# Performance work log

Measured on AMD Instinct MI355X. Metric: run time of the kernel, lower is better.

Reference implementation:

```python
import jax, jax.numpy as jnp
import numpy as np

EMBED_DIM = 768
N_HEADS = 12
HEAD_DIM = EMBED_DIM // N_HEADS


def setup_inputs() -> dict:
    key = jax.random.key(0)
    ks = jax.random.split(key, 6)
    bsz, seq = 2, 4096
    hidden_states = jax.random.normal(ks[0], (bsz, seq, EMBED_DIM), dtype=jnp.float32)
    attention_mask = jnp.zeros((bsz, 1, 1, seq), dtype=jnp.float32)
    s = 1.0 / np.sqrt(EMBED_DIM)
    Wq = jax.random.normal(ks[1], (EMBED_DIM, EMBED_DIM), dtype=jnp.float32) * s
    Wk = jax.random.normal(ks[2], (EMBED_DIM, EMBED_DIM), dtype=jnp.float32) * s
    Wv = jax.random.normal(ks[3], (EMBED_DIM, EMBED_DIM), dtype=jnp.float32) * s
    Wo = jax.random.normal(ks[4], (EMBED_DIM, EMBED_DIM), dtype=jnp.float32) * s
    bo = jax.random.normal(ks[5], (EMBED_DIM,), dtype=jnp.float32) * s
    return {"hidden_states": hidden_states, "attention_mask": attention_mask,
            "Wq": Wq, "Wk": Wk, "Wv": Wv, "Wo": Wo, "bo": bo}


def reference(hidden_states, attention_mask, Wq, Wk, Wv, Wo, bo):
    bsz, seq, _ = hidden_states.shape
    scale = 1.0 / np.sqrt(HEAD_DIM)

    def split_heads(x):  # [b, s, e] -> [b, h, s, d]
        return x.reshape(bsz, seq, N_HEADS, HEAD_DIM).transpose(0, 2, 1, 3)

    # nn.Linear applies x @ W.T
    q = split_heads(hidden_states @ Wq.T)
    k = split_heads(hidden_states @ Wk.T)
    v = split_heads(hidden_states @ Wv.T)

    # [b, h, tgt, src] score matrix (faithful to the bmm+softmax+bmm original)
    attn = jnp.einsum('bhqd,bhkd->bhqk', q, k) * scale
    attn = attn + attention_mask  # mask broadcasts [b,1,1,src]
    probs = jax.nn.softmax(attn, axis=-1)
    ctx = jnp.einsum('bhqk,bhkd->bhqd', probs, v)

    concat = ctx.transpose(0, 2, 1, 3).reshape(bsz, seq, EMBED_DIM)
    return concat @ Wo.T + bo
```

## Files before the change

### kernel.cpp

```cpp
#include <hip/hip_runtime.h>
#include <stdint.h>

#define ED   768
#define NH   12
#define HD   64
#define SEQ  4096
#define BSZ  2
#define BHT  (BSZ*NH)
#define MTOT (BSZ*SEQ)

typedef short bf16x8  __attribute__((ext_vector_type(8)));
typedef float f32x4   __attribute__((ext_vector_type(4)));
typedef float f32x16  __attribute__((ext_vector_type(16)));
typedef unsigned int u32x4 __attribute__((ext_vector_type(4)));

#define LOG2E 1.44269504088896340736f
#define C2    (0.125f * LOG2E)

__device__ __forceinline__ unsigned short f2bf(float f) {
    union { float f; uint32_t u; } v; v.f = f;
    uint32_t u = v.u;
    u += 0x7fffu + ((u >> 16) & 1u);
    return (unsigned short)(u >> 16);
}

__device__ __forceinline__ uint32_t cvtpk(float lo, float hi) {
    uint32_t r;
    asm("v_cvt_pk_bf16_f32 %0, %1, %2" : "=v"(r) : "v"(lo), "v"(hi));
    return r;
}

__device__ __forceinline__ void cp16(const unsigned short* g, unsigned short* l) {
    __builtin_amdgcn_global_load_lds(
        (const __attribute__((address_space(1))) unsigned int*)(const void*)g,
        (__attribute__((address_space(3))) unsigned int*)(void*)l,
        16, 0, 0);
}

#define H_CHUNKS  (MTOT * ED / 4)
#define W_CHUNKS  (ED * ED / 4)
#define CVT_TOTAL (H_CHUNKS + 4 * W_CHUNKS)

__global__ __launch_bounds__(256) void convert_bf16(
    const float* __restrict__ H,  const float* __restrict__ Wq,
    const float* __restrict__ Wk, const float* __restrict__ Wv,
    const float* __restrict__ Wo, unsigned short* __restrict__ dst,
    unsigned short* __restrict__ WoB) {
    int i4 = blockIdx.x * 256 + threadIdx.x;
    float4 v;
    ushort4* optr;
    if (i4 < H_CHUNKS) { v = ((const float4*)H)[i4]; optr = (ushort4*)dst + i4; }
    else {
        int j = i4 - H_CHUNKS;
        if (j < 3 * W_CHUNKS) {
            if (j < W_CHUNKS)          v = ((const float4*)Wq)[j];
            else if (j < 2 * W_CHUNKS) v = ((const float4*)Wk)[j - W_CHUNKS];
            else                       v = ((const float4*)Wv)[j - 2 * W_CHUNKS];
            optr = (ushort4*)dst + i4;
        } else {
            v = ((const float4*)Wo)[j - 3 * W_CHUNKS];
            optr = (ushort4*)WoB + (j - 3 * W_CHUNKS);
        }
    }
    ushort4 o;
    o.x = f2bf(v.x); o.y = f2bf(v.y); o.z = f2bf(v.z); o.w = f2bf(v.w);
    *optr = o;
}

__global__ __launch_bounds__(256) void qkv_gemm(
    const unsigned short* __restrict__ Hb,
    const unsigned short* __restrict__ Wb,
    unsigned short* __restrict__ qkv) {
    __shared__ __align__(16) unsigned short Ah[128 * 64];
    __shared__ __align__(16) unsigned short Bh[128 * 64];
    const int t = threadIdx.x, w = t >> 6, lane = t & 63;
    const int quad = lane >> 4, r16 = lane & 15;
    const int wm = w >> 1, wn = w & 1;
    const int m0 = blockIdx.y * 128, n0g = blockIdx.x * 128;
    const int wsel = n0g / ED, n0 = n0g % ED;
    const int lrow = lane >> 3;
    const int lchs = ((lane & 7) ^ (lrow & 7)) * 8;

    f32x4 acc[4][4] = {};
    for (int kt = 0; kt < ED / 64; ++kt) {
        const int k0 = kt * 64;
#pragma unroll
        for (int i = 0; i < 4; ++i) {
            int row = i * 32 + w * 8;
            cp16(&Hb[(size_t)(m0 + row + lrow) * ED + k0 + lchs], &Ah[row * 64]);
            cp16(&Wb[(size_t)(n0g + row + lrow) * ED + k0 + lchs], &Bh[row * 64]);
        }
        __syncthreads();
#pragma unroll
        for (int kk = 0; kk < 2; ++kk) {
            bf16x8 aF[4], bF[4];
#pragma unroll
            for (int mi = 0; mi < 4; ++mi) {
                int R = wm * 64 + mi * 16 + r16;
                aF[mi] = *(const bf16x8*)&Ah[R * 64 + (((kk * 4 + quad) ^ (r16 & 7)) * 8)];
            }
#pragma unroll
            for (int ni = 0; ni < 4; ++ni) {
                int R = wn * 64 + ni * 16 + r16;
                bF[ni] = *(const bf16x8*)&Bh[R * 64 + (((kk * 4 + quad) ^ (r16 & 7)) * 8)];
            }
            if (wsel == 2) {
#pragma unroll
                for (int mi = 0; mi < 4; ++mi)
#pragma unroll
                    for (int ni = 0; ni < 4; ++ni)
                        acc[mi][ni] = __builtin_amdgcn_mfma_f32_16x16x32_bf16(
                            bF[ni], aF[mi], acc[mi][ni], 0, 0, 0);
            } else {
#pragma unroll
                for (int mi = 0; mi < 4; ++mi)
#pragma unroll
                    for (int ni = 0; ni < 4; ++ni)
                        acc[mi][ni] = __builtin_amdgcn_mfma_f32_16x16x32_bf16(
                            aF[mi], bF[ni], acc[mi][ni], 0, 0, 0);
            }
        }
        __syncthreads();
    }
    const size_t WSZ = (size_t)BHT * SEQ * HD;
    if (wsel == 2) {
#pragma unroll
        for (int mi = 0; mi < 4; ++mi)
#pragma unroll
            for (int ni = 0; ni < 4; ++ni)
#pragma unroll
                for (int r = 0; r < 4; ++r) {
                    int m  = m0 + wm * 64 + mi * 16 + r16;
                    int nn = n0 + wn * 64 + ni * 16 + quad * 4 + r;
                    int b = m >> 12, s = m & 4095;
                    int hh = nn >> 6, dd = nn & 63;
                    qkv[2 * WSZ + (((size_t)b * NH + hh) * HD + dd) * SEQ + s] =
                        f2bf(acc[mi][ni][r]);
                }
    } else {
        const float sc = (wsel == 0) ? C2 : 1.0f;
#pragma unroll
        for (int mi = 0; mi < 4; ++mi)
#pragma unroll
            for (int ni = 0; ni < 4; ++ni)
#pragma unroll
                for (int r = 0; r < 4; ++r) {
                    int m = m0 + wm * 64 + mi * 16 + quad * 4 + r;
                    int b = m >> 12, s = m & 4095;
                    int nn = n0 + wn * 64 + ni * 16 + r16;
                    int hh = nn >> 6, dd = nn & 63;
                    size_t off = (((size_t)b * NH + hh) * SEQ + s) * HD + dd;
                    qkv[(size_t)wsel * WSZ + off] = f2bf(acc[mi][ni][r] * sc);
                }
    }
}

#define QK_PACK(KOFF, M0, M1, PF) do {                                         \
    float p_[2][16];                                                           \
    float rs0 = 0.f, rs1 = 0.f, rs2 = 0.f, rs3 = 0.f;                          \
_Pragma("unroll")                                                              \
    for (int st = 0; st < 2; ++st) {                                           \
        bf16x8 am = {};                                                        \
        if (hi == 0) am[0] = (short)f2bf(LOG2E * (st ? (M1) : (M0)));          \
        f32x16 sA = {};                                                        \
        sA = __builtin_amdgcn_mfma_f32_32x32x16_bf16(am, bOnes, sA, 0, 0, 0);  \
        __builtin_amdgcn_s_setprio(1);                                         \
_Pragma("unroll")                                                              \
        for (int kc = 0; kc < 4; ++kc) {                                       \
            bf16x8 kF = *(const bf16x8*)                                       \
                &Ksm[(KOFF) + (st * 32 + n31) * 64 + (((2 * kc + hi) ^ sw) * 8)]; \
            sA = __builtin_amdgcn_mfma_f32_32x32x16_bf16(kF, qF[kc], sA, 0, 0, 0); \
        }                                                                      \
        __builtin_amdgcn_s_setprio(0);                                         \
_Pragma("unroll")                                                              \
        for (int r = 0; r < 16; ++r) p_[st][r] = __builtin_amdgcn_exp2f(sA[r]); \
        rs0 += p_[st][0] + p_[st][4] + p_[st][8]  + p_[st][12];                \
        rs1 += p_[st][1] + p_[st][5] + p_[st][9]  + p_[st][13];                \
        rs2 += p_[st][2] + p_[st][6] + p_[st][10] + p_[st][14];                \
        rs3 += p_[st][3] + p_[st][7] + p_[st][11] + p_[st][15];                \
    }                                                                          \
    l_i += (rs0 + rs1) + (rs2 + rs3);                                          \
_Pragma("unroll")                                                              \
    for (int st = 0; st < 2; ++st) {                                           \
        uint32_t pw[8];                                                        \
_Pragma("unroll")                                                              \
        for (int i = 0; i < 8; ++i)                                            \
            pw[i] = cvtpk(p_[st][2 * i], p_[st][2 * i + 1]);                   \
_Pragma("unroll")                                                              \
        for (int hf = 0; hf < 2; ++hf) {                                       \
            auto r02 = __builtin_amdgcn_permlane32_swap(                       \
                pw[hf * 4 + 0], pw[hf * 4 + 2], false, false);                 \
            auto r13 = __builtin_amdgcn_permlane32_swap(                       \
                pw[hf * 4 + 1], pw[hf * 4 + 3], false, false);                 \
            union { u32x4 u; bf16x8 h; } f_;                                   \
            f_.u[0] = r02[0]; f_.u[1] = r13[0]; f_.u[2] = r02[1]; f_.u[3] = r13[1]; \
            PF[st * 2 + hf] = f_.h;                                            \
        }                                                                      \
    }                                                                          \
} while (0)

#define PV_ACC(VOFF, PF) do {                                                  \
    __builtin_amdgcn_s_setprio(1);                                             \
_Pragma("unroll")                                                              \
    for (int kc = 0; kc < 4; ++kc) {                                           \
_Pragma("unroll")                                                              \
        for (int dt = 0; dt < 2; ++dt) {                                       \
            bf16x8 vF = *(const bf16x8*)                                       \
                &Vtsm[(VOFF) + (dt * 32 + n31) * 64 + (((2 * kc + hi) ^ sw) * 8)]; \
            oAcc[dt] = __builtin_amdgcn_mfma_f32_32x32x16_bf16(                \
                vF, PF[kc], oAcc[dt], 0, 0, 0);                                \
        }                                                                      \
    }                                                                          \
    __builtin_amdgcn_s_setprio(0);                                             \
} while (0)

__global__ __launch_bounds__(256) void flash_attn(
    const unsigned short* __restrict__ qkv, const float* __restrict__ mask,
    unsigned short* __restrict__ ctx) {
    __shared__ __align__(16) unsigned short Ksm[3 * 4096];
    __shared__ __align__(16) unsigned short Vtsm[2 * 4096];
    const int t  = threadIdx.x;
    const int bh = blockIdx.y;
    const int b  = bh / NH;
    const int h  = bh % NH;
    const int qbase = blockIdx.x * 128;
    const size_t WSZ = (size_t)BHT * SEQ * HD;
    const unsigned short* Qp = qkv + (size_t)bh * SEQ * HD;
    const unsigned short* Kp = Qp + WSZ;
    const unsigned short* Vt = qkv + 2 * WSZ + (size_t)bh * HD * SEQ;
    const int w = t >> 6, lane = t & 63, n31 = lane & 31, hi = lane >> 5;
    const int lrow = lane >> 3;
    const int lchs = ((lane & 7) ^ (lrow & 7)) * 8;

    bf16x8 qF[4];
    {
        int qrow = qbase + w * 32 + n31;
#pragma unroll
        for (int kc = 0; kc < 4; ++kc)
            qF[kc] = *(const bf16x8*)&Qp[(size_t)qrow * HD + kc * 16 + hi * 8];
    }
    bf16x8 bOnes = {};
    if (hi == 0) bOnes[0] = (short)0x3F80;

    const float* mrow = mask + (size_t)b * SEQ;
    float mReg0 = mrow[n31], mReg1 = mrow[32 + n31];

    const int row0 = w * 16, row1 = w * 16 + 8;

    cp16(&Kp[(size_t)(row0 + lrow) * HD + lchs],      &Ksm[row0 * 64]);
    cp16(&Kp[(size_t)(row1 + lrow) * HD + lchs],      &Ksm[row1 * 64]);
    cp16(&Kp[(size_t)(64 + row0 + lrow) * HD + lchs], &Ksm[4096 + row0 * 64]);
    cp16(&Kp[(size_t)(64 + row1 + lrow) * HD + lchs], &Ksm[4096 + row1 * 64]);
    cp16(&Vt[(size_t)(row0 + lrow) * SEQ + lchs],     &Vtsm[row0 * 64]);
    cp16(&Vt[(size_t)(row1 + lrow) * SEQ + lchs],     &Vtsm[row1 * 64]);
    __syncthreads();

    f32x16 oAcc[2] = {};
    float l_i = 0.0f;
    const int sw = n31 & 7;
    int kCur = 0, kNxt = 4096, kFar = 8192;
    int vCur = 0;

    for (int kt = 0; kt < 62; ++kt) {
        float mN0 = mrow[(kt + 1) * 64 + n31];
        float mN1 = mrow[(kt + 1) * 64 + 32 + n31];
        cp16(&Kp[(size_t)((kt + 2) * 64 + row0 + lrow) * HD + lchs], &Ksm[kFar + row0 * 64]);
        cp16(&Kp[(size_t)((kt + 2) * 64 + row1 + lrow) * HD + lchs], &Ksm[kFar + row1 * 64]);
        cp16(&Vt[(size_t)(row0 + lrow) * SEQ + (kt + 1) * 64 + lchs], &Vtsm[(vCur ^ 4096) + row0 * 64]);
        cp16(&Vt[(size_t)(row1 + lrow) * SEQ + (kt + 1) * 64 + lchs], &Vtsm[(vCur ^ 4096) + row1 * 64]);

        bf16x8 pF[4];
        QK_PACK(kCur, mReg0, mReg1, pF);
        asm volatile("s_waitcnt vmcnt(4)\n\ts_barrier" ::: "memory");
        PV_ACC(vCur, pF);
        asm volatile("s_barrier" ::: "memory");

        int tmp = kCur; kCur = kNxt; kNxt = kFar; kFar = tmp;
        vCur ^= 4096;
        mReg0 = mN0; mReg1 = mN1;
    }
    {
        float mN0 = mrow[63 * 64 + n31];
        float mN1 = mrow[63 * 64 + 32 + n31];
        cp16(&Vt[(size_t)(row0 + lrow) * SEQ + 63 * 64 + lchs], &Vtsm[(vCur ^ 4096) + row0 * 64]);
        cp16(&Vt[(size_t)(row1 + lrow) * SEQ + 63 * 64 + lchs], &Vtsm[(vCur ^ 4096) + row1 * 64]);
        bf16x8 pF[4];
        QK_PACK(kCur, mReg0, mReg1, pF);
        asm volatile("s_waitcnt vmcnt(2)\n\ts_barrier" ::: "memory");
        PV_ACC(vCur, pF);
        asm volatile("s_barrier" ::: "memory");
        int tmp = kCur; kCur = kNxt; kNxt = kFar; kFar = tmp;
        vCur ^= 4096;
        mReg0 = mN0; mReg1 = mN1;
    }
    {
        bf16x8 pF[4];
        QK_PACK(kCur, mReg0, mReg1, pF);
        asm volatile("s_waitcnt vmcnt(0)\n\ts_barrier" ::: "memory");
        PV_ACC(vCur, pF);
    }

    l_i += __shfl_xor(l_i, 32);
    float inv = 1.0f / l_i;
    int s = qbase + w * 32 + n31;
    unsigned short* obase = &ctx[((size_t)b * SEQ + s) * ED + h * HD];
#pragma unroll
    for (int dt = 0; dt < 2; ++dt)
#pragma unroll
        for (int g = 0; g < 4; ++g) {
            ushort4 o;
            o.x = f2bf(oAcc[dt][4 * g + 0] * inv);
            o.y = f2bf(oAcc[dt][4 * g + 1] * inv);
            o.z = f2bf(oAcc[dt][4 * g + 2] * inv);
            o.w = f2bf(oAcc[dt][4 * g + 3] * inv);
            *(ushort4*)&obase[dt * 32 + hi * 4 + 8 * g] = o;
        }
}

__global__ __launch_bounds__(256) void out_gemm(
    const unsigned short* __restrict__ Ab,
    const unsigned short* __restrict__ Wob,
    const float* __restrict__ bo, float* __restrict__ out) {
    __shared__ __align__(16) unsigned short Ah[128 * 64];
    __shared__ __align__(16) unsigned short Bh[128 * 64];
    const int t = threadIdx.x, w = t >> 6, lane = t & 63;
    const int quad = lane >> 4, r16 = lane & 15;
    const int wm = w >> 1, wn = w & 1;
    const int m0 = blockIdx.y * 128, n0 = blockIdx.x * 128;
    const int lrow = lane >> 3;
    const int lchs = ((lane & 7) ^ (lrow & 7)) * 8;

    f32x4 acc[4][4] = {};
    for (int kt = 0; kt < ED / 64; ++kt) {
        const int k0 = kt * 64;
#pragma unroll
        for (int i = 0; i < 4; ++i) {
            int row = i * 32 + w * 8;
            cp16(&Ab[(size_t)(m0 + row + lrow) * ED + k0 + lchs], &Ah[row * 64]);
            cp16(&Wob[(size_t)(n0 + row + lrow) * ED + k0 + lchs], &Bh[row * 64]);
        }
        __syncthreads();
#pragma unroll
        for (int kk = 0; kk < 2; ++kk) {
            bf16x8 aF[4], bF[4];
#pragma unroll
            for (int mi = 0; mi < 4; ++mi) {
                int R = wm * 64 + mi * 16 + r16;
                aF[mi] = *(const bf16x8*)&Ah[R * 64 + (((kk * 4 + quad) ^ (r16 & 7)) * 8)];
            }
#pragma unroll
            for (int ni = 0; ni < 4; ++ni) {
                int R = wn * 64 + ni * 16 + r16;
                bF[ni] = *(const bf16x8*)&Bh[R * 64 + (((kk * 4 + quad) ^ (r16 & 7)) * 8)];
            }
#pragma unroll
            for (int mi = 0; mi < 4; ++mi)
#pragma unroll
                for (int ni = 0; ni < 4; ++ni)
                    acc[mi][ni] = __builtin_amdgcn_mfma_f32_16x16x32_bf16(
                        aF[mi], bF[ni], acc[mi][ni], 0, 0, 0);
        }
        __syncthreads();
    }
    float bov[4];
#pragma unroll
    for (int ni = 0; ni < 4; ++ni) bov[ni] = bo[n0 + wn * 64 + ni * 16 + r16];
#pragma unroll
    for (int mi = 0; mi < 4; ++mi)
#pragma unroll
        for (int ni = 0; ni < 4; ++ni)
#pragma unroll
            for (int r = 0; r < 4; ++r) {
                int m = m0 + wm * 64 + mi * 16 + quad * 4 + r;
                int n = n0 + wn * 64 + ni * 16 + r16;
                out[(size_t)m * ED + n] = acc[mi][ni][r] + bov[ni];
            }
}

extern "C" void kernel_launch(void* const* d_in, const int* in_sizes, int n_in,
                              void* d_out, int out_size, void* d_ws, size_t ws_size,
                              hipStream_t stream) {
    const float* H    = (const float*)d_in[0];
    const float* mask = (const float*)d_in[1];
    const float* Wq   = (const float*)d_in[2];
    const float* Wk   = (const float*)d_in[3];
    const float* Wv   = (const float*)d_in[4];
    const float* Wo   = (const float*)d_in[5];
    const float* bo   = (const float*)d_in[6];
    unsigned short* ws = (unsigned short*)d_ws;
    const size_t WSZ = (size_t)BHT * SEQ * HD;
    unsigned short* qkv = ws;
    unsigned short* ctx = ws + 3 * WSZ;
    unsigned short* WoB = ctx + (size_t)MTOT * ED;
    float* out = (float*)d_out;
    unsigned short* Hb = (unsigned short*)d_out;
    unsigned short* Wb = Hb + (size_t)MTOT * ED;

    convert_bf16<<<CVT_TOTAL / 256, 256, 0, stream>>>(H, Wq, Wk, Wv, Wo, Hb, WoB);
    qkv_gemm<<<dim3(3 * ED / 128, MTOT / 128), 256, 0, stream>>>(Hb, Wb, qkv);
    flash_attn<<<dim3(SEQ / 128, BHT), 256, 0, stream>>>(qkv, mask, ctx);
    out_gemm<<<dim3(ED / 128, MTOT / 128), 256, 0, stream>>>(ctx, WoB, bo, out);
}
```

Before: 291.3 us.

## Software-pipeline flash attention: overlap next tile's QK MFMA with current PV

Restructures the flash-attention main loop so each iteration issues the QK^T MFMAs for the next key tile together with the PV MFMAs for the current tile. The exp/pack softmax work for the next tile then runs after that MFMA burst. The aim is to hide exp2 and permlane VALU latency behind matrix-core work and to give the MFMA pipe a longer uninterrupted stream. In exchange it holds more live registers (two score accumulators plus the previous P fragments), changes the wait counts and prologue/epilogue, and may lower occupancy.

Result: slower. 318.4 us (+9.3%).

```diff
diff --git a/kernel.cpp b/kernel.cpp
--- a/kernel.cpp
+++ b/kernel.cpp
@@ -155,37 +155,54 @@
     }
 }
 
-#define QK_PACK(KOFF, M0, M1, PF) do {                                         \
-    float p_[2][16];                                                           \
-    float rs0 = 0.f, rs1 = 0.f, rs2 = 0.f, rs3 = 0.f;                          \
+#define QK_MFMA(KOFF, M0, M1) do {                                             \
+    bf16x8 am0 = {}, am1 = {};                                                 \
+    if (hi == 0) { am0[0] = (short)f2bf(LOG2E * (M0));                         \
+                   am1[0] = (short)f2bf(LOG2E * (M1)); }                       \
+    sA0 = __builtin_amdgcn_mfma_f32_32x32x16_bf16(am0, bOnes, Z, 0, 0, 0);     \
+    sA1 = __builtin_amdgcn_mfma_f32_32x32x16_bf16(am1, bOnes, Z, 0, 0, 0);     \
+_Pragma("unroll")                                                              \
+    for (int kc = 0; kc < 4; ++kc) {                                           \
+        bf16x8 kF = *(const bf16x8*)                                           \
+            &Ksm[(KOFF) + n31 * 64 + (((2 * kc + hi) ^ sw) * 8)];              \
+        sA0 = __builtin_amdgcn_mfma_f32_32x32x16_bf16(kF, qF[kc], sA0, 0, 0, 0); \
+    }                                                                          \
+_Pragma("unroll")                                                              \
+    for (int kc = 0; kc < 4; ++kc) {                                           \
+        bf16x8 kF = *(const bf16x8*)                                           \
+            &Ksm[(KOFF) + (32 + n31) * 64 + (((2 * kc + hi) ^ sw) * 8)];       \
+        sA1 = __builtin_amdgcn_mfma_f32_32x32x16_bf16(kF, qF[kc], sA1, 0, 0, 0); \
+    }                                                                          \
+} while (0)
+
+#define PV_MFMA(VOFF, PF) do {                                                 \
+_Pragma("unroll")                                                              \
+    for (int kc = 0; kc < 4; ++kc) {                                           \
+_Pragma("unroll")                                                              \
+        for (int dt = 0; dt < 2; ++dt) {                                       \
+            bf16x8 vF = *(const bf16x8*)                                       \
+                &Vtsm[(VOFF) + (dt * 32 + n31) * 64 + (((2 * kc + hi) ^ sw) * 8)]; \
+            oAcc[dt] = __builtin_amdgcn_mfma_f32_32x32x16_bf16(                \
+                vF, PF[kc], oAcc[dt], 0, 0, 0);                                \
+        }                                                                      \
+    }                                                                          \
+} while (0)
+
+#define SM_PACK(PF_OUT) do {                                                   \
 _Pragma("unroll")                                                              \
     for (int st = 0; st < 2; ++st) {                                           \
-        bf16x8 am = {};                                                        \
-        if (hi == 0) am[0] = (short)f2bf(LOG2E * (st ? (M1) : (M0)));          \
-        f32x16 sA = {};                                                        \
-        sA = __builtin_amdgcn_mfma_f32_32x32x16_bf16(am, bOnes, sA, 0, 0, 0);  \
-        __builtin_amdgcn_s_setprio(1);                                         \
-_Pragma("unroll")                                                              \
-        for (int kc = 0; kc < 4; ++kc) {                                       \
-            bf16x8 kF = *(const bf16x8*)                                       \
-                &Ksm[(KOFF) + (st * 32 + n31) * 64 + (((2 * kc + hi) ^ sw) * 8)]; \
-            sA = __builtin_amdgcn_mfma_f32_32x32x16_bf16(kF, qF[kc], sA, 0, 0, 0); \
-        }                                                                      \
-        __builtin_amdgcn_s_setprio(0);                                         \
-_Pragma("unroll")                                                              \
-        for (int r = 0; r < 16; ++r) p_[st][r] = __builtin_amdgcn_exp2f(sA[r]); \
-        rs0 += p_[st][0] + p_[st][4] + p_[st][8]  + p_[st][12];                \
-        rs1 += p_[st][1] + p_[st][5] + p_[st][9]  + p_[st][13];                \
-        rs2 += p_[st][2] + p_[st][6] + p_[st][10] + p_[st][14];                \
-        rs3 += p_[st][3] + p_[st][7] + p_[st][11] + p_[st][15];                \
-    }                                                                          \
-    l_i += (rs0 + rs1) + (rs2 + rs3);                                          \
-_Pragma("unroll")                                                              \
-    for (int st = 0; st < 2; ++st) {                                           \
+        float p_[16];                                                          \
+        const f32x16& sA = st ? sA1 : sA0;                                     \
+_Pragma("unroll")                                                              \
+        for (int r = 0; r < 16; ++r) p_[r] = __builtin_amdgcn_exp2f(sA[r]);    \
+        l_i += (((p_[0] + p_[1]) + (p_[2] + p_[3])) +                          \
+                ((p_[4] + p_[5]) + (p_[6] + p_[7]))) +                         \
+               (((p_[8] + p_[9]) + (p_[10] + p_[11])) +                        \
+                ((p_[12] + p_[13]) + (p_[14] + p_[15])));                      \
         uint32_t pw[8];                                                        \
 _Pragma("unroll")                                                              \
         for (int i = 0; i < 8; ++i)                                            \
-            pw[i] = cvtpk(p_[st][2 * i], p_[st][2 * i + 1]);                   \
+            pw[i] = cvtpk(p_[2 * i], p_[2 * i + 1]);                           \
 _Pragma("unroll")                                                              \
         for (int hf = 0; hf < 2; ++hf) {                                       \
             auto r02 = __builtin_amdgcn_permlane32_swap(                       \
@@ -194,24 +211,9 @@
                 pw[hf * 4 + 1], pw[hf * 4 + 3], false, false);                 \
             union { u32x4 u; bf16x8 h; } f_;                                   \
             f_.u[0] = r02[0]; f_.u[1] = r13[0]; f_.u[2] = r02[1]; f_.u[3] = r13[1]; \
-            PF[st * 2 + hf] = f_.h;                                            \
+            PF_OUT[st * 2 + hf] = f_.h;                                        \
         }                                                                      \
     }                                                                          \
-} while (0)
-
-#define PV_ACC(VOFF, PF) do {                                                  \
-    __builtin_amdgcn_s_setprio(1);                                             \
-_Pragma("unroll")                                                              \
-    for (int kc = 0; kc < 4; ++kc) {                                           \
-_Pragma("unroll")                                                              \
-        for (int dt = 0; dt < 2; ++dt) {                                       \
-            bf16x8 vF = *(const bf16x8*)                                       \
-                &Vtsm[(VOFF) + (dt * 32 + n31) * 64 + (((2 * kc + hi) ^ sw) * 8)]; \
-            oAcc[dt] = __builtin_amdgcn_mfma_f32_32x32x16_bf16(                \
-                vF, PF[kc], oAcc[dt], 0, 0, 0);                                \
-        }                                                                      \
-    }                                                                          \
-    __builtin_amdgcn_s_setprio(0);                                             \
 } while (0)
 
 __global__ __launch_bounds__(256) void flash_attn(
@@ -241,10 +243,9 @@
     }
     bf16x8 bOnes = {};
     if (hi == 0) bOnes[0] = (short)0x3F80;
+    const f32x16 Z = {};
 
     const float* mrow = mask + (size_t)b * SEQ;
-    float mReg0 = mrow[n31], mReg1 = mrow[32 + n31];
-
     const int row0 = w * 16, row1 = w * 16 + 8;
 
     cp16(&Kp[(size_t)(row0 + lrow) * HD + lchs],      &Ksm[row0 * 64]);
@@ -253,6 +254,8 @@
     cp16(&Kp[(size_t)(64 + row1 + lrow) * HD + lchs], &Ksm[4096 + row1 * 64]);
     cp16(&Vt[(size_t)(row0 + lrow) * SEQ + lchs],     &Vtsm[row0 * 64]);
     cp16(&Vt[(size_t)(row1 + lrow) * SEQ + lchs],     &Vtsm[row1 * 64]);
+    float m00 = mrow[n31],      m01 = mrow[32 + n31];
+    float mA0 = mrow[64 + n31], mA1 = mrow[96 + n31];
     __syncthreads();
 
     f32x16 oAcc[2] = {};
@@ -261,43 +264,52 @@
     int kCur = 0, kNxt = 4096, kFar = 8192;
     int vCur = 0;
 
+    bf16x8 pFA[4];
+    {
+        f32x16 sA0, sA1;
+        QK_MFMA(0, m00, m01);
+        SM_PACK(pFA);
+    }
+
     for (int kt = 0; kt < 62; ++kt) {
-        float mN0 = mrow[(kt + 1) * 64 + n31];
-        float mN1 = mrow[(kt + 1) * 64 + 32 + n31];
+        float mN0 = mrow[(kt + 2) * 64 + n31];
+        float mN1 = mrow[(kt + 2) * 64 + 32 + n31];
         cp16(&Kp[(size_t)((kt + 2) * 64 + row0 + lrow) * HD + lchs], &Ksm[kFar + row0 * 64]);
         cp16(&Kp[(size_t)((kt + 2) * 64 + row1 + lrow) * HD + lchs], &Ksm[kFar + row1 * 64]);
         cp16(&Vt[(size_t)(row0 + lrow) * SEQ + (kt + 1) * 64 + lchs], &Vtsm[(vCur ^ 4096) + row0 * 64]);
         cp16(&Vt[(size_t)(row1 + lrow) * SEQ + (kt + 1) * 64 + lchs], &Vtsm[(vCur ^ 4096) + row1 * 64]);
 
-        bf16x8 pF[4];
-        QK_PACK(kCur, mReg0, mReg1, pF);
-        asm volatile("s_waitcnt vmcnt(4)\n\ts_barrier" ::: "memory");
-        PV_ACC(vCur, pF);
+        asm volatile("s_waitcnt vmcnt(6)\n\ts_barrier" ::: "memory");
+
+        f32x16 sA0, sA1;
+        __builtin_amdgcn_s_setprio(1);
+        QK_MFMA(kNxt, mA0, mA1);
+        PV_MFMA(vCur, pFA);
+        __builtin_amdgcn_s_setprio(0);
+
+        bf16x8 pFB[4];
+        SM_PACK(pFB);
+
         asm volatile("s_barrier" ::: "memory");
 
         int tmp = kCur; kCur = kNxt; kNxt = kFar; kFar = tmp;
         vCur ^= 4096;
-        mReg0 = mN0; mReg1 = mN1;
+        mA0 = mN0; mA1 = mN1;
+        pFA[0] = pFB[0]; pFA[1] = pFB[1]; pFA[2] = pFB[2]; pFA[3] = pFB[3];
     }
     {
-        float mN0 = mrow[63 * 64 + n31];
-        float mN1 = mrow[63 * 64 + 32 + n31];
         cp16(&Vt[(size_t)(row0 + lrow) * SEQ + 63 * 64 + lchs], &Vtsm[(vCur ^ 4096) + row0 * 64]);
         cp16(&Vt[(size_t)(row1 + lrow) * SEQ + 63 * 64 + lchs], &Vtsm[(vCur ^ 4096) + row1 * 64]);
-        bf16x8 pF[4];
-        QK_PACK(kCur, mReg0, mReg1, pF);
         asm volatile("s_waitcnt vmcnt(2)\n\ts_barrier" ::: "memory");
-        PV_ACC(vCur, pF);
-        asm volatile("s_barrier" ::: "memory");
-        int tmp = kCur; kCur = kNxt; kNxt = kFar; kFar = tmp;
-        vCur ^= 4096;
-        mReg0 = mN0; mReg1 = mN1;
-    }
-    {
-        bf16x8 pF[4];
-        QK_PACK(kCur, mReg0, mReg1, pF);
+        f32x16 sA0, sA1;
+        __builtin_amdgcn_s_setprio(1);
+        QK_MFMA(kNxt, mA0, mA1);
+        PV_MFMA(vCur, pFA);
+        __builtin_amdgcn_s_setprio(0);
+        bf16x8 pFB[4];
+        SM_PACK(pFB);
         asm volatile("s_waitcnt vmcnt(0)\n\ts_barrier" ::: "memory");
-        PV_ACC(vCur, pF);
+        PV_MFMA(vCur ^ 4096, pFB);
     }
 
     l_i += __shfl_xor(l_i, 32);
```
